# Optimization experiments

Measured on AMD Instinct MI355X. Metric: run time of the kernel, lower is better.

Reference implementation:

```python
import jax, jax.numpy as jnp
import numpy as np

B, T, H = 16, 2048, 1024   # batch, time, hidden_dim
G, V, D = 2, 320, 128      # num_codebooks, codebook_size, codebook_dim
TAU = 1.0                  # gumbel-softmax temperature (forward default)
EPS = 1e-9


def setup_inputs() -> dict:
    key = jax.random.key(0)
    ks = jax.random.split(key, 6)
    return {
        "x": jax.random.normal(ks[0], (B, T, H), jnp.float32),
        "W_in": jax.random.normal(ks[1], (G * V, H), jnp.float32) / np.sqrt(H),
        "b_in": jnp.zeros((G * V,), jnp.float32),
        "codebook": jax.random.uniform(ks[2], (G, V, D), jnp.float32),
        "W_out": jax.random.normal(ks[3], (H, G * D), jnp.float32) / np.sqrt(G * D),
        "b_out": jnp.zeros((H,), jnp.float32),
        "gumbel_u": jax.random.uniform(ks[4], (B, T, G, V), jnp.float32,
                                       minval=1e-6, maxval=1.0 - 1e-6),
    }


def reference(x, W_in, b_in, codebook, W_out, b_out, gumbel_u):
    # input projection -> per-group logits [B,T,G,V]
    logits = (x @ W_in.T + b_in).reshape(B, T, G, V)
    # gumbel-softmax (soft, training path)
    gumbels = -jnp.log(-jnp.log(gumbel_u))
    probs = jax.nn.softmax((logits + gumbels) / TAU, axis=-1)
    # perplexity over average code usage
    avg_probs = probs.mean(axis=(0, 1))  # [G,V]
    perplexity = jnp.exp(-(avg_probs * jnp.log(avg_probs + EPS)).sum(-1)).mean()
    # quantize: soft mixture over codebook, concat groups, project out
    q = jnp.einsum('btgv,gvd->btgd', probs, codebook).reshape(B, T, G * D)
    q = q @ W_out.T + b_out  # [B,T,H]
    commit_loss = jnp.mean((x - jax.lax.stop_gradient(q)) ** 2)
    return (q, perplexity, commit_loss)
```

## Files before the change

### kernel.cpp

```cpp
#include <hip/hip_runtime.h>

typedef unsigned short ushort_t;
typedef unsigned int uint_t;
typedef __attribute__((ext_vector_type(4))) float f32x4;
typedef __attribute__((ext_vector_type(8))) short bf16x8;

#define B_   16
#define T_   2048
#define H_   1024
#define G_   2
#define V_   320
#define D_   128
#define NT   32768
#define GV   640
#define GD   256

__device__ __forceinline__ ushort_t cvt_bf16(float f) {
  uint_t u = __float_as_uint(f);
  uint_t r = (u + 0x7FFFu + ((u >> 16) & 1u)) >> 16;
  return (ushort_t)r;
}

__global__ void pq_prep(const float* __restrict__ W_in, const float* __restrict__ W_out,
                        const float* __restrict__ cb, ushort_t* __restrict__ winb,
                        ushort_t* __restrict__ woutb, ushort_t* __restrict__ cbp,
                        float* __restrict__ avg_g, float* __restrict__ closs) {
  int idx = blockIdx.x * 256 + threadIdx.x;
  const int N1 = GV * H_;
  const int N2 = H_ * GD;
  const int N3 = 81920;
  if (idx < N1) { winb[idx] = cvt_bf16(W_in[idx]); return; }
  idx -= N1;
  if (idx < N2) { woutb[idx] = cvt_bf16(W_out[idx]); return; }
  idx -= N2;
  if (idx < N3) {
    int g = idx / 40960;
    int r = idx % 40960;
    int kk = r / 4096;
    int r2 = r % 4096;
    int n  = r2 >> 9;
    int ln = (r2 >> 3) & 63;
    int i  = r2 & 7;
    int v = kk * 32 + (ln >> 4) * 8 + i;
    int d = n * 16 + (ln & 15);
    cbp[idx] = cvt_bf16(cb[((size_t)g * V_ + v) * D_ + d]);
    return;
  }
  idx -= N3;
  if (idx < GV) { avg_g[idx] = 0.f; return; }
  idx -= GV;
  if (idx == 0) *closs = 0.f;
}

__global__ __launch_bounds__(512, 2) void pq_kA(
    const float* __restrict__ x, const float* __restrict__ b_in,
    const float* __restrict__ gum, const ushort_t* __restrict__ winb,
    const ushort_t* __restrict__ cbp, ushort_t* __restrict__ qmid,
    float* __restrict__ avg_g) {
  __shared__ char smem[84480];
  char* sA = smem;
  char* sB = smem + 8192;
  char* sP = smem;
  float* sAvg = (float*)(smem + 81920);

  const int tid = threadIdx.x;
  const int lane = tid & 63;
  const int wid = tid >> 6;
  const int wm = wid >> 1;
  const int g  = wid & 1;
  const int lo = lane & 15;
  const int hi = lane >> 4;
  const int row0 = blockIdx.x * 128;

  for (int i = tid; i < GV; i += 512) sAvg[i] = 0.f;

  f32x4 acc[2][20];
#pragma unroll
  for (int m = 0; m < 2; ++m)
#pragma unroll
    for (int n = 0; n < 20; ++n) acc[m][n] = (f32x4){0.f, 0.f, 0.f, 0.f};

  __syncthreads();

  for (int ks = 0; ks < 32; ++ks) {
    const int kb = ks * 32;
#pragma unroll
    for (int u = 0; u < 2; ++u) {
      int f = u * 512 + tid;
      int r = f >> 3, c4 = f & 7;
      const float4 xv = *reinterpret_cast<const float4*>(x + (size_t)(row0 + r) * H_ + kb + c4 * 4);
      uint2 w;
      w.x = (uint_t)cvt_bf16(xv.x) | ((uint_t)cvt_bf16(xv.y) << 16);
      w.y = (uint_t)cvt_bf16(xv.z) | ((uint_t)cvt_bf16(xv.w) << 16);
      int byte = (r * 64 + c4 * 8) ^ ((r & 7) << 4);
      *reinterpret_cast<uint2*>(sA + byte) = w;
    }
#pragma unroll
    for (int u = 0; u < 5; ++u) {
      int s = u * 512 + tid;
      int r = s >> 2, c = s & 3;
      const uint4 wv = *reinterpret_cast<const uint4*>(winb + (size_t)r * H_ + kb + c * 8);
      int byte = (r * 64 + c * 16) ^ ((r & 7) << 4);
      *reinterpret_cast<uint4*>(sB + byte) = wv;
    }
    __syncthreads();
    bf16x8 af[2];
#pragma unroll
    for (int m = 0; m < 2; ++m) {
      int row = wm * 32 + m * 16 + lo;
      int byte = (row * 64 + hi * 16) ^ ((row & 7) << 4);
      af[m] = *reinterpret_cast<const bf16x8*>(sA + byte);
    }
#pragma unroll
    for (int n = 0; n < 20; ++n) {
      int v = g * 320 + n * 16 + lo;
      int byte = (v * 64 + hi * 16) ^ ((v & 7) << 4);
      bf16x8 bf = *reinterpret_cast<const bf16x8*>(sB + byte);
      acc[0][n] = __builtin_amdgcn_mfma_f32_16x16x32_bf16(af[0], bf, acc[0][n], 0, 0, 0);
      acc[1][n] = __builtin_amdgcn_mfma_f32_16x16x32_bf16(af[1], bf, acc[1][n], 0, 0, 0);
    }
    __syncthreads();
  }

  float bias[20];
#pragma unroll
  for (int n = 0; n < 20; ++n) bias[n] = b_in[g * 320 + n * 16 + lo];

#pragma unroll
  for (int mrep = 0; mrep < 2; ++mrep) {
#pragma unroll
    for (int j = 0; j < 4; ++j) {
      const int trow = row0 + wm * 32 + mrep * 16 + hi * 4 + j;
      const float* up = gum + ((size_t)trow * G_ + g) * V_;
      float zmax = -3.0e38f;
#pragma unroll
      for (int n = 0; n < 20; ++n) {
        float u = up[n * 16 + lo];
        float gv = -__logf(-__logf(u));
        float z = acc[mrep][n][j] + bias[n] + gv;
        acc[mrep][n][j] = z;
        zmax = fmaxf(zmax, z);
      }
#pragma unroll
      for (int mk = 1; mk <= 8; mk <<= 1) zmax = fmaxf(zmax, __shfl_xor(zmax, mk));
      float s = 0.f;
#pragma unroll
      for (int n = 0; n < 20; ++n) {
        float p = __expf(acc[mrep][n][j] - zmax);
        acc[mrep][n][j] = p;
        s += p;
      }
#pragma unroll
      for (int mk = 1; mk <= 8; mk <<= 1) s += __shfl_xor(s, mk);
      float inv = 1.f / s;
#pragma unroll
      for (int n = 0; n < 20; ++n) acc[mrep][n][j] *= inv;
    }
#pragma unroll
    for (int n = 0; n < 20; ++n) {
      float cs = acc[mrep][n][0] + acc[mrep][n][1] + acc[mrep][n][2] + acc[mrep][n][3];
      cs += __shfl_xor(cs, 16);
      cs += __shfl_xor(cs, 32);
      if (hi == 0) atomicAdd(&sAvg[g * 320 + n * 16 + lo], cs);
    }
#pragma unroll
    for (int n = 0; n < 20; ++n) {
#pragma unroll
      for (int j = 0; j < 4; ++j) {
        float v = acc[mrep][n][j];
        float pv = __shfl_xor(v, 1);
        if ((lane & 1) == 0) {
          uint_t w = (uint_t)cvt_bf16(v) | ((uint_t)cvt_bf16(pv) << 16);
          int prow = wm * 16 + hi * 4 + j;
          int byte = (prow * 1280 + (g * 320 + n * 16 + lo) * 2) ^ ((prow & 7) << 4);
          *reinterpret_cast<uint_t*>(sP + byte) = w;
        }
      }
    }
    asm volatile("s_waitcnt lgkmcnt(0)" ::: "memory");
    f32x4 acc2[8];
#pragma unroll
    for (int n = 0; n < 8; ++n) acc2[n] = (f32x4){0.f, 0.f, 0.f, 0.f};
#pragma unroll
    for (int kk = 0; kk < 10; ++kk) {
      int prow = wm * 16 + lo;
      int byte = (prow * 1280 + g * 640 + kk * 64 + hi * 16) ^ ((prow & 7) << 4);
      bf16x8 ap = *reinterpret_cast<const bf16x8*>(sP + byte);
#pragma unroll
      for (int n = 0; n < 8; ++n) {
        bf16x8 bc = *reinterpret_cast<const bf16x8*>(cbp + ((size_t)((g * 10 + kk) * 8 + n) * 64 + lane) * 8);
        acc2[n] = __builtin_amdgcn_mfma_f32_16x16x32_bf16(ap, bc, acc2[n], 0, 0, 0);
      }
    }
#pragma unroll
    for (int n = 0; n < 8; ++n) {
#pragma unroll
      for (int j = 0; j < 4; ++j) {
        float v = acc2[n][j];
        float pv = __shfl_xor(v, 1);
        if ((lane & 1) == 0) {
          uint_t w = (uint_t)cvt_bf16(v) | ((uint_t)cvt_bf16(pv) << 16);
          int trow = row0 + wm * 32 + mrep * 16 + hi * 4 + j;
          *reinterpret_cast<uint_t*>(qmid + (size_t)trow * GD + g * 128 + n * 16 + lo) = w;
        }
      }
    }
  }
  __syncthreads();
  for (int i = tid; i < GV; i += 512) atomicAdd(&avg_g[i], sAvg[i]);
}

__global__ __launch_bounds__(512, 2) void pq_kB(
    const ushort_t* __restrict__ qmid, const ushort_t* __restrict__ woutb,
    const float* __restrict__ b_out, const float* __restrict__ x,
    float* __restrict__ out, float* __restrict__ closs) {
  __shared__ char smem[49152 + 64];
  char* sA = smem;
  char* sB = smem + 16384;
  float* sRed = (float*)(smem + 49152);

  const int tid = threadIdx.x;
  const int lane = tid & 63;
  const int wid = tid >> 6;
  const int wm = wid >> 2;
  const int wn = wid & 3;
  const int lo = lane & 15, hi = lane >> 4;
  const int tm = blockIdx.x >> 2;
  const int tn = blockIdx.x & 3;
  const int row0 = tm * 128;
  const int col0 = tn * 256;

  f32x4 acc[4][4];
#pragma unroll
  for (int mr = 0; mr < 4; ++mr)
#pragma unroll
    for (int nr = 0; nr < 4; ++nr) acc[mr][nr] = (f32x4){0.f, 0.f, 0.f, 0.f};

  for (int ks = 0; ks < 4; ++ks) {
    const int kb = ks * 64;
#pragma unroll
    for (int u = 0; u < 2; ++u) {
      int s = u * 512 + tid;
      int r = s >> 3, c = s & 7;
      uint4 wv = *reinterpret_cast<const uint4*>(qmid + (size_t)(row0 + r) * GD + kb + c * 8);
      int byte = (r * 128 + c * 16) ^ ((r & 7) << 4);
      *reinterpret_cast<uint4*>(sA + byte) = wv;
    }
#pragma unroll
    for (int u = 0; u < 4; ++u) {
      int s = u * 512 + tid;
      int r = s >> 3, c = s & 7;
      uint4 wv = *reinterpret_cast<const uint4*>(woutb + (size_t)(col0 + r) * GD + kb + c * 8);
      int byte = (r * 128 + c * 16) ^ ((r & 7) << 4);
      *reinterpret_cast<uint4*>(sB + byte) = wv;
    }
    __syncthreads();
#pragma unroll
    for (int kk = 0; kk < 2; ++kk) {
      bf16x8 af[4], bf[4];
#pragma unroll
      for (int mr = 0; mr < 4; ++mr) {
        int row = wm * 64 + mr * 16 + lo;
        int byte = (row * 128 + kk * 64 + hi * 16) ^ ((row & 7) << 4);
        af[mr] = *reinterpret_cast<const bf16x8*>(sA + byte);
      }
#pragma unroll
      for (int nr = 0; nr < 4; ++nr) {
        int col = wn * 64 + nr * 16 + lo;
        int byte = (col * 128 + kk * 64 + hi * 16) ^ ((col & 7) << 4);
        bf[nr] = *reinterpret_cast<const bf16x8*>(sB + byte);
      }
#pragma unroll
      for (int mr = 0; mr < 4; ++mr)
#pragma unroll
        for (int nr = 0; nr < 4; ++nr)
          acc[mr][nr] = __builtin_amdgcn_mfma_f32_16x16x32_bf16(af[mr], bf[nr], acc[mr][nr], 0, 0, 0);
    }
    __syncthreads();
  }
  float bias[4];
#pragma unroll
  for (int nr = 0; nr < 4; ++nr) bias[nr] = b_out[col0 + wn * 64 + nr * 16 + lo];
  float csum = 0.f;
#pragma unroll
  for (int mr = 0; mr < 4; ++mr)
#pragma unroll
    for (int nr = 0; nr < 4; ++nr)
#pragma unroll
      for (int j = 0; j < 4; ++j) {
        int row = row0 + wm * 64 + mr * 16 + hi * 4 + j;
        int col = col0 + wn * 64 + nr * 16 + lo;
        float q = acc[mr][nr][j] + bias[nr];
        out[(size_t)row * H_ + col] = q;
        float d = x[(size_t)row * H_ + col] - q;
        csum += d * d;
      }
#pragma unroll
  for (int mk = 1; mk <= 32; mk <<= 1) csum += __shfl_xor(csum, mk);
  if (lane == 0) sRed[wid] = csum;
  __syncthreads();
  if (tid == 0) {
    float t = 0.f;
    for (int w = 0; w < 8; ++w) t += sRed[w];
    atomicAdd(closs, t);
  }
}

__global__ void pq_kC(const float* __restrict__ avg_g, const float* __restrict__ closs,
                      float* __restrict__ out) {
  const int lane = threadIdx.x;
  float a0 = 0.f, a1 = 0.f;
  for (int v = lane; v < V_; v += 64) {
    float p0 = avg_g[v] * (1.f / (float)NT);
    a0 += p0 * __logf(p0 + 1e-9f);
    float p1 = avg_g[V_ + v] * (1.f / (float)NT);
    a1 += p1 * __logf(p1 + 1e-9f);
  }
#pragma unroll
  for (int mk = 1; mk <= 32; mk <<= 1) { a0 += __shfl_xor(a0, mk); a1 += __shfl_xor(a1, mk); }
  if (lane == 0) {
    out[(size_t)NT * H_]     = 0.5f * (__expf(-a0) + __expf(-a1));
    out[(size_t)NT * H_ + 1] = (*closs) * (1.f / ((float)NT * (float)H_));
  }
}

extern "C" void kernel_launch(void* const* d_in, const int* in_sizes, int n_in,
                              void* d_out, int out_size, void* d_ws, size_t ws_size,
                              hipStream_t stream) {
  const float* x     = (const float*)d_in[0];
  const float* W_in  = (const float*)d_in[1];
  const float* b_in  = (const float*)d_in[2];
  const float* cb    = (const float*)d_in[3];
  const float* W_out = (const float*)d_in[4];
  const float* b_out = (const float*)d_in[5];
  const float* gum   = (const float*)d_in[6];
  float* out = (float*)d_out;

  char* ws = (char*)d_ws;
  ushort_t* winb  = (ushort_t*)ws;
  ushort_t* woutb = (ushort_t*)(ws + 1310720);
  ushort_t* cbp   = (ushort_t*)(ws + 1835008);
  float*    avg_g = (float*)(ws + 1998848);
  float*    closs = (float*)(ws + 2001408);
  ushort_t* qmid  = (ushort_t*)(ws + 2001920);

  pq_prep<<<3907, 256, 0, stream>>>(W_in, W_out, cb, winb, woutb, cbp, avg_g, closs);
  pq_kA<<<256, 512, 0, stream>>>(x, b_in, gum, winb, cbp, qmid, avg_g);
  pq_kB<<<1024, 512, 0, stream>>>(qmid, woutb, b_out, x, out, closs);
  pq_kC<<<1, 64, 0, stream>>>(avg_g, closs, out);
}
```

Before: 204.0 us.

## Register-prefetch next K tile in projection GEMM and fold finalize into last block

The input-projection GEMM loop now loads the next K-slice of x and W_in into registers before the MFMA work on the current slice, so global-load latency overlaps compute. The two syncthreads per iteration become explicit lgkmcnt waits plus raw barriers. Separately, the tiny perplexity/commit-loss finalize kernel is removed: kB blocks increment a global counter, and the last block computes the scalars, which saves one launch. This costs extra registers in an already register-heavy kernel and relies on a threadfence/atomic pattern for correctness.

```diff
diff --git a/kernel.cpp b/kernel.cpp
--- a/kernel.cpp
+++ b/kernel.cpp
@@ -15,6 +15,9 @@
 #define GV   640
 #define GD   256
 
+#define LGKM0() asm volatile("s_waitcnt lgkmcnt(0)" ::: "memory")
+#define BAR()   __builtin_amdgcn_s_barrier()
+
 __device__ __forceinline__ ushort_t cvt_bf16(float f) {
   uint_t u = __float_as_uint(f);
   uint_t r = (u + 0x7FFFu + ((u >> 16) & 1u)) >> 16;
@@ -24,7 +27,8 @@
 __global__ void pq_prep(const float* __restrict__ W_in, const float* __restrict__ W_out,
                         const float* __restrict__ cb, ushort_t* __restrict__ winb,
                         ushort_t* __restrict__ woutb, ushort_t* __restrict__ cbp,
-                        float* __restrict__ avg_g, float* __restrict__ closs) {
+                        float* __restrict__ avg_g, float* __restrict__ closs,
+                        uint_t* __restrict__ counter) {
   int idx = blockIdx.x * 256 + threadIdx.x;
   const int N1 = GV * H_;
   const int N2 = H_ * GD;
@@ -49,7 +53,7 @@
   idx -= N3;
   if (idx < GV) { avg_g[idx] = 0.f; return; }
   idx -= GV;
-  if (idx == 0) *closs = 0.f;
+  if (idx == 0) { *closs = 0.f; *counter = 0u; }
 }
 
 __global__ __launch_bounds__(512, 2) void pq_kA(
@@ -74,6 +78,17 @@
 
   for (int i = tid; i < GV; i += 512) sAvg[i] = 0.f;
 
+  const int ar0 = tid >> 3;
+  const int ac4 = tid & 7;
+  const float* aptr0 = x + (size_t)(row0 + ar0) * H_ + ac4 * 4;
+  const float* aptr1 = aptr0 + (size_t)64 * H_;
+  const int abyte0 = (ar0 * 64 + ac4 * 8) ^ ((ar0 & 7) << 4);
+
+  const int br0 = tid >> 2;
+  const int bc  = tid & 3;
+  const ushort_t* bptr0 = winb + (size_t)br0 * H_ + bc * 8;
+  const int bbyte0 = (br0 * 64 + bc * 16) ^ ((br0 & 7) << 4);
+
   f32x4 acc[2][20];
 #pragma unroll
   for (int m = 0; m < 2; ++m)
@@ -82,44 +97,50 @@
 
   __syncthreads();
 
+  float4 ra0 = *reinterpret_cast<const float4*>(aptr0);
+  float4 ra1 = *reinterpret_cast<const float4*>(aptr1);
+  uint4 rb[5];
+#pragma unroll
+  for (int u = 0; u < 5; ++u)
+    rb[u] = *reinterpret_cast<const uint4*>(bptr0 + (size_t)u * 128 * H_);
+
+#pragma unroll 1
   for (int ks = 0; ks < 32; ++ks) {
-    const int kb = ks * 32;
-#pragma unroll
-    for (int u = 0; u < 2; ++u) {
-      int f = u * 512 + tid;
-      int r = f >> 3, c4 = f & 7;
-      const float4 xv = *reinterpret_cast<const float4*>(x + (size_t)(row0 + r) * H_ + kb + c4 * 4);
-      uint2 w;
-      w.x = (uint_t)cvt_bf16(xv.x) | ((uint_t)cvt_bf16(xv.y) << 16);
-      w.y = (uint_t)cvt_bf16(xv.z) | ((uint_t)cvt_bf16(xv.w) << 16);
-      int byte = (r * 64 + c4 * 8) ^ ((r & 7) << 4);
-      *reinterpret_cast<uint2*>(sA + byte) = w;
-    }
-#pragma unroll
-    for (int u = 0; u < 5; ++u) {
-      int s = u * 512 + tid;
-      int r = s >> 2, c = s & 3;
-      const uint4 wv = *reinterpret_cast<const uint4*>(winb + (size_t)r * H_ + kb + c * 8);
-      int byte = (r * 64 + c * 16) ^ ((r & 7) << 4);
-      *reinterpret_cast<uint4*>(sB + byte) = wv;
-    }
-    __syncthreads();
-    bf16x8 af[2];
-#pragma unroll
-    for (int m = 0; m < 2; ++m) {
-      int row = wm * 32 + m * 16 + lo;
-      int byte = (row * 64 + hi * 16) ^ ((row & 7) << 4);
-      af[m] = *reinterpret_cast<const bf16x8*>(sA + byte);
-    }
+    uint2 w0, w1;
+    w0.x = (uint_t)cvt_bf16(ra0.x) | ((uint_t)cvt_bf16(ra0.y) << 16);
+    w0.y = (uint_t)cvt_bf16(ra0.z) | ((uint_t)cvt_bf16(ra0.w) << 16);
+    w1.x = (uint_t)cvt_bf16(ra1.x) | ((uint_t)cvt_bf16(ra1.y) << 16);
+    w1.y = (uint_t)cvt_bf16(ra1.z) | ((uint_t)cvt_bf16(ra1.w) << 16);
+    *reinterpret_cast<uint2*>(sA + abyte0) = w0;
+    *reinterpret_cast<uint2*>(sA + abyte0 + 4096) = w1;
+#pragma unroll
+    for (int u = 0; u < 5; ++u)
+      *reinterpret_cast<uint4*>(sB + bbyte0 + u * 8192) = rb[u];
+
+    if (ks < 31) {
+      const int ko = (ks + 1) * 32;
+      ra0 = *reinterpret_cast<const float4*>(aptr0 + ko);
+      ra1 = *reinterpret_cast<const float4*>(aptr1 + ko);
+#pragma unroll
+      for (int u = 0; u < 5; ++u)
+        rb[u] = *reinterpret_cast<const uint4*>(bptr0 + (size_t)u * 128 * H_ + ko);
+    }
+
+    LGKM0();
+    BAR();
+
+    const int rowm = wm * 32 + lo;
+    bf16x8 af0 = *reinterpret_cast<const bf16x8*>(sA + ((rowm * 64 + hi * 16) ^ ((rowm & 7) << 4)));
+    bf16x8 af1 = *reinterpret_cast<const bf16x8*>(sA + ((rowm * 64 + hi * 16) ^ ((rowm & 7) << 4)) + 1024);
 #pragma unroll
     for (int n = 0; n < 20; ++n) {
       int v = g * 320 + n * 16 + lo;
-      int byte = (v * 64 + hi * 16) ^ ((v & 7) << 4);
-      bf16x8 bf = *reinterpret_cast<const bf16x8*>(sB + byte);
-      acc[0][n] = __builtin_amdgcn_mfma_f32_16x16x32_bf16(af[0], bf, acc[0][n], 0, 0, 0);
-      acc[1][n] = __builtin_amdgcn_mfma_f32_16x16x32_bf16(af[1], bf, acc[1][n], 0, 0, 0);
-    }
-    __syncthreads();
+      bf16x8 bf = *reinterpret_cast<const bf16x8*>(sB + ((v * 64 + hi * 16) ^ ((v & 7) << 4)));
+      acc[0][n] = __builtin_amdgcn_mfma_f32_16x16x32_bf16(af0, bf, acc[0][n], 0, 0, 0);
+      acc[1][n] = __builtin_amdgcn_mfma_f32_16x16x32_bf16(af1, bf, acc[1][n], 0, 0, 0);
+    }
+    LGKM0();
+    BAR();
   }
 
   float bias[20];
@@ -177,7 +198,7 @@
         }
       }
     }
-    asm volatile("s_waitcnt lgkmcnt(0)" ::: "memory");
+    LGKM0();
     f32x4 acc2[8];
 #pragma unroll
     for (int n = 0; n < 8; ++n) acc2[n] = (f32x4){0.f, 0.f, 0.f, 0.f};
@@ -213,8 +234,10 @@
 __global__ __launch_bounds__(512, 2) void pq_kB(
     const ushort_t* __restrict__ qmid, const ushort_t* __restrict__ woutb,
     const float* __restrict__ b_out, const float* __restrict__ x,
-    float* __restrict__ out, float* __restrict__ closs) {
+    float* __restrict__ out, float* __restrict__ closs,
+    const float* __restrict__ avg_g, uint_t* __restrict__ counter) {
   __shared__ char smem[49152 + 64];
+  __shared__ int sLast;
   char* sA = smem;
   char* sB = smem + 16384;
   float* sRed = (float*)(smem + 49152);
@@ -303,24 +326,26 @@
     float t = 0.f;
     for (int w = 0; w < 8; ++w) t += sRed[w];
     atomicAdd(closs, t);
-  }
-}
-
-__global__ void pq_kC(const float* __restrict__ avg_g, const float* __restrict__ closs,
-                      float* __restrict__ out) {
-  const int lane = threadIdx.x;
-  float a0 = 0.f, a1 = 0.f;
-  for (int v = lane; v < V_; v += 64) {
-    float p0 = avg_g[v] * (1.f / (float)NT);
-    a0 += p0 * __logf(p0 + 1e-9f);
-    float p1 = avg_g[V_ + v] * (1.f / (float)NT);
-    a1 += p1 * __logf(p1 + 1e-9f);
-  }
-#pragma unroll
-  for (int mk = 1; mk <= 32; mk <<= 1) { a0 += __shfl_xor(a0, mk); a1 += __shfl_xor(a1, mk); }
-  if (lane == 0) {
-    out[(size_t)NT * H_]     = 0.5f * (__expf(-a0) + __expf(-a1));
-    out[(size_t)NT * H_ + 1] = (*closs) * (1.f / ((float)NT * (float)H_));
+    __threadfence();
+    uint_t c = atomicAdd(counter, 1u);
+    sLast = (c == 1023u) ? 1 : 0;
+  }
+  __syncthreads();
+  if (sLast && tid < 64) {
+    float a0 = 0.f, a1 = 0.f;
+    for (int v = tid; v < V_; v += 64) {
+      float p0 = avg_g[v] * (1.f / (float)NT);
+      a0 += p0 * __logf(p0 + 1e-9f);
+      float p1 = avg_g[V_ + v] * (1.f / (float)NT);
+      a1 += p1 * __logf(p1 + 1e-9f);
+    }
+#pragma unroll
+    for (int mk = 1; mk <= 32; mk <<= 1) { a0 += __shfl_xor(a0, mk); a1 += __shfl_xor(a1, mk); }
+    if (tid == 0) {
+      float cl = atomicAdd(closs, 0.0f);
+      out[(size_t)NT * H_]     = 0.5f * (__expf(-a0) + __expf(-a1));
+      out[(size_t)NT * H_ + 1] = cl * (1.f / ((float)NT * (float)H_));
+    }
   }
 }
 
@@ -342,10 +367,10 @@
   ushort_t* cbp   = (ushort_t*)(ws + 1835008);
   float*    avg_g = (float*)(ws + 1998848);
   float*    closs = (float*)(ws + 2001408);
+  uint_t*   cnt   = (uint_t*)(ws + 2001472);
   ushort_t* qmid  = (ushort_t*)(ws + 2001920);
 
-  pq_prep<<<3907, 256, 0, stream>>>(W_in, W_out, cb, winb, woutb, cbp, avg_g, closs);
+  pq_prep<<<3907, 256, 0, stream>>>(W_in, W_out, cb, winb, woutb, cbp, avg_g, closs, cnt);
   pq_kA<<<256, 512, 0, stream>>>(x, b_in, gum, winb, cbp, qmid, avg_g);
-  pq_kB<<<1024, 512, 0, stream>>>(qmid, woutb, b_out, x, out, closs);
-  pq_kC<<<1, 64, 0, stream>>>(avg_g, closs, out);
-}
+  pq_kB<<<1024, 512, 0, stream>>>(qmid, woutb, b_out, x, out, closs, avg_g, cnt);
+}
```

Result: slower. 287.4 us (+40.9%).
